# Performance work log

Hardware: AMD Instinct MI355X
Metric: run time of the kernel (lower is better)

The kernel has to match this reference:

```python
import jax, jax.numpy as jnp
import numpy as np

K = 5          # kernel_size per pseudo-dim
KK = K * K     # 25 weight slots (dim=2)
NUM_GRAPHS = 64


def spline_conv(x, src, dst, pseudo, W, root, bias):
    """SplineConv, degree-1 open B-spline, dim=2, aggr='mean', root weight + bias.
    x: [N, I], pseudo: [E, 2] in [0,1], W: [KK, I, O], root: [I, O], bias: [O].
    """
    N = x.shape[0]
    E = src.shape[0]
    O = W.shape[-1]
    # degree-1 open spline: v = u * (K-1); linear interpolation between knots
    v = pseudo * (K - 1)                      # [E, 2]
    bot = jnp.floor(v)
    frac = v - bot                            # [E, 2]
    bot = bot.astype(jnp.int32)
    # precompute per-node transform for every kernel slot: [N, KK, O] -> flat [N*KK, O]
    Xk = jnp.einsum('ni,kio->nko', x, W).reshape(N * KK, O)
    msg = jnp.zeros((E, O), x.dtype)
    for s0 in (0, 1):
        b0 = frac[:, 0] if s0 else 1.0 - frac[:, 0]
        i0 = jnp.clip(bot[:, 0] + s0, 0, K - 1)
        for s1 in (0, 1):
            b1 = frac[:, 1] if s1 else 1.0 - frac[:, 1]
            i1 = jnp.clip(bot[:, 1] + s1, 0, K - 1)
            flat = src * KK + i0 * K + i1     # [E] gather index into Xk
            msg = msg + (b0 * b1)[:, None] * Xk[flat]
    # mean aggregation over incoming edges
    agg = jax.ops.segment_sum(msg, dst, num_segments=N)
    deg = jax.ops.segment_sum(jnp.ones((E,), x.dtype), dst, num_segments=N)
    agg = agg / jnp.maximum(deg, 1.0)[:, None]
    return agg + x @ root + bias


def batch_average(x, batch, num_graphs):
    s = jax.ops.segment_sum(x, batch, num_segments=num_graphs)
    c = jax.ops.segment_sum(jnp.ones((x.shape[0],), x.dtype), batch, num_segments=num_graphs)
    return s / jnp.maximum(c, 1.0)[:, None]


def setup_inputs() -> dict:
    key = jax.random.key(0)
    ks = jax.random.split(key, 16)
    N, E = 30000, 600000
    x = jax.random.normal(ks[0], (N, 8), dtype=jnp.float32)
    edge_index = jax.random.randint(ks[1], (2, E), 0, N, dtype=jnp.int64)
    pseudo = jax.random.uniform(ks[2], (E, 2), dtype=jnp.float32)
    batch = jnp.sort(jax.random.randint(ks[3], (N,), 0, NUM_GRAPHS, dtype=jnp.int64))

    def glorot(k, shape):
        fan = shape[-2] + shape[-1]
        return jax.random.normal(k, shape, dtype=jnp.float32) * np.sqrt(2.0 / fan)

    return {
        'x': x, 'edge_index': edge_index, 'pseudo': pseudo, 'batch': batch,
        'W1': glorot(ks[4], (KK, 8, 32)),   'root1': glorot(ks[5], (8, 32)),   'b1': jnp.zeros((32,), jnp.float32),
        'W2': glorot(ks[6], (KK, 32, 64)),  'root2': glorot(ks[7], (32, 64)),  'b2': jnp.zeros((64,), jnp.float32),
        'W3': glorot(ks[8], (KK, 64, 124)), 'root3': glorot(ks[9], (64, 124)), 'b3': jnp.zeros((124,), jnp.float32),
        'fc_w': glorot(ks[10], (124, 30)),  'fc_b': jnp.zeros((30,), jnp.float32),
    }


def reference(x, edge_index, pseudo, batch,
              W1, root1, b1, W2, root2, b2, W3, root3, b3, fc_w, fc_b):
    src = edge_index[0].astype(jnp.int32)
    dst = edge_index[1].astype(jnp.int32)
    batch32 = batch.astype(jnp.int32)
    h = jax.nn.elu(spline_conv(x, src, dst, pseudo, W1, root1, b1))
    h = jax.nn.elu(spline_conv(h, src, dst, pseudo, W2, root2, b2))
    h = jax.nn.elu(spline_conv(h, src, dst, pseudo, W3, root3, b3))
    g = batch_average(h, batch32, NUM_GRAPHS)        # [G, 124]
    # dropout is identity in eval mode
    logits = g @ fc_w + fc_b                         # [G, 30]
    return jax.nn.log_softmax(logits, axis=-1)
```

## Files before the change

kernel.cpp:

```cpp
#include <hip/hip_runtime.h>
#include <cstdint>
#include <cstddef>

#define KKSLOTS 25

typedef __attribute__((ext_vector_type(8))) short short8;
typedef __attribute__((ext_vector_type(4))) float f32x4;
typedef __attribute__((ext_vector_type(4))) unsigned short us4;

__device__ __forceinline__ unsigned short f2bf(float f) {
    unsigned u = __float_as_uint(f);
    u += 0x7FFF + ((u >> 16) & 1);
    return (unsigned short)(u >> 16);
}
__device__ __forceinline__ float bf2f(unsigned short b) {
    return __uint_as_float((unsigned)b << 16);
}

__global__ void csr_count_kernel(const int* __restrict__ dst, int* __restrict__ cnt, int E) {
    int e = blockIdx.x * blockDim.x + threadIdx.x;
    if (e < E) atomicAdd(&cnt[dst[e]], 1);
}

#define SCAN_B 256
__global__ __launch_bounds__(SCAN_B) void scan1_kernel(const int* __restrict__ cnt,
                                                       int* __restrict__ off,
                                                       int* __restrict__ bsum, int N) {
    __shared__ int tmp[SCAN_B];
    int g = blockIdx.x * SCAN_B + threadIdx.x;
    int v = (g < N) ? cnt[g] : 0;
    tmp[threadIdx.x] = v;
    __syncthreads();
    for (int d = 1; d < SCAN_B; d <<= 1) {
        int t = (threadIdx.x >= d) ? tmp[threadIdx.x - d] : 0;
        __syncthreads();
        tmp[threadIdx.x] += t;
        __syncthreads();
    }
    if (g < N) off[g] = tmp[threadIdx.x] - v;
    if (threadIdx.x == SCAN_B - 1) bsum[blockIdx.x] = tmp[threadIdx.x];
}

__global__ __launch_bounds__(SCAN_B) void scan2_kernel(int* __restrict__ bsum, int nb) {
    __shared__ int tmp[SCAN_B];
    int v = (threadIdx.x < nb) ? bsum[threadIdx.x] : 0;
    tmp[threadIdx.x] = v;
    __syncthreads();
    for (int d = 1; d < SCAN_B; d <<= 1) {
        int t = (threadIdx.x >= d) ? tmp[threadIdx.x - d] : 0;
        __syncthreads();
        tmp[threadIdx.x] += t;
        __syncthreads();
    }
    if (threadIdx.x < nb) bsum[threadIdx.x] = tmp[threadIdx.x] - v;
}

__global__ void scan3_kernel(int* __restrict__ off, const int* __restrict__ bsum, int N) {
    int g = blockIdx.x * SCAN_B + threadIdx.x;
    if (g < N) off[g] += bsum[blockIdx.x];
}

__global__ void csr_fill_kernel(const int* __restrict__ src, const int* __restrict__ dst,
                                const float* __restrict__ pseudo,
                                int* __restrict__ off, int4* __restrict__ rec, int E) {
    int e = blockIdx.x * blockDim.x + threadIdx.x;
    if (e >= E) return;
    int d = dst[e];
    int p = atomicAdd(&off[d], 1);
    float v0 = pseudo[2 * e + 0] * 4.0f;
    float v1 = pseudo[2 * e + 1] * 4.0f;
    float fl0 = floorf(v0), fl1 = floorf(v1);
    float f0 = v0 - fl0, f1 = v1 - fl1;
    int b0 = (int)fl0, b1 = (int)fl1;
    int i0a = min(max(b0, 0), 4),     i1a = min(max(b1, 0), 4);
    int i0b = min(max(b0 + 1, 0), 4), i1b = min(max(b1 + 1, 0), 4);
    int s00 = i0a * 5 + i1a;
    int s01 = i0a * 5 + i1b;
    int s10 = i0b * 5 + i1a;
    int s11 = i0b * 5 + i1b;
    int packed = s00 | (s01 << 5) | (s10 << 10) | (s11 << 15);
    int4 r;
    r.x = src[e];
    r.y = packed;
    r.z = __float_as_int(f0);
    r.w = __float_as_int(f1);
    rec[p] = r;
}

__global__ void to_bf16_kernel(const float* __restrict__ in, unsigned short* __restrict__ out, int n) {
    int i = blockIdx.x * 256 + threadIdx.x;
    if (i < n) out[i] = f2bf(in[i]);
}

template<int KP, int I, int O, int OP>
__global__ void build_wt_kernel(const float* __restrict__ W, const float* __restrict__ root,
                                unsigned short* __restrict__ WT) {
    int idx = blockIdx.x * 256 + threadIdx.x;
    if (idx >= OP * KP) return;
    int o = idx / KP, k = idx - o * KP;
    float v = 0.0f;
    if (o < O) {
        if (k < KKSLOTS * I) v = W[(size_t)k * O + o];
        else if (k < (KKSLOTS + 1) * I) v = root[(size_t)(k - KKSLOTS * I) * O + o];
    }
    WT[idx] = f2bf(v);
}

template<int I>
__device__ __forceinline__ void edge_add(float* la, int lane, int4 r,
                                         const unsigned short* __restrict__ xb) {
    float f0 = __int_as_float(r.z), f1 = __int_as_float(r.w);
    float g0 = 1.0f - f0, g1 = 1.0f - f1;
    int pk = r.y;
    if constexpr (I == 64) {
        float xv = bf2f(xb[(size_t)r.x * 64 + lane]);
        la[((pk      ) & 31) * 64 + lane] += g0 * g1 * xv;
        la[((pk >> 5 ) & 31) * 64 + lane] += g0 * f1 * xv;
        la[((pk >> 10) & 31) * 64 + lane] += f0 * g1 * xv;
        la[((pk >> 15) & 31) * 64 + lane] += f0 * f1 * xv;
    } else if constexpr (I == 32) {
        int ch = lane & 31, half = lane >> 5;
        float xv = bf2f(xb[(size_t)r.x * 32 + ch]);
        float wA = half ? f0 : g0;
        int sh = half * 10;
        int sA = (pk >> sh) & 31, sB = (pk >> (sh + 5)) & 31;
        la[sA * 32 + ch] += wA * g1 * xv;
        la[sB * 32 + ch] += wA * f1 * xv;
    } else {
        int ch = lane & 7, corner = (lane >> 3) & 3;
        if (lane < 32) {
            float xv = bf2f(xb[(size_t)r.x * 8 + ch]);
            int s = (pk >> (corner * 5)) & 31;
            float w = ((corner & 2) ? f0 : g0) * ((corner & 1) ? f1 : g1);
            la[s * 8 + ch] += w * xv;
        }
    }
}

template<int I, int KP>
__global__ __launch_bounds__(256) void seg_accum_kernel(
        const unsigned short* __restrict__ xb, const int4* __restrict__ rec,
        const int* __restrict__ off, unsigned short* __restrict__ accB,
        int nlo, int nhi) {
    constexpr int SLOTS = KKSLOTS * I;
    __shared__ float la_all[4][SLOTS];
    int wline = threadIdx.x >> 6, lane = threadIdx.x & 63;
    float* la = la_all[wline];
    int wid = blockIdx.x * 4 + wline;
    int nwt = gridDim.x << 2;

    int e_lo = (nlo == 0) ? 0 : off[nlo - 1];
    int e_hi = off[nhi - 1];
    long long span = (long long)e_hi - e_lo;
    int t0 = e_lo + (int)(span * wid / nwt);
    int t1 = e_lo + (int)(span * (wid + 1) / nwt);

    int ns, ne;
    {   int lo = nlo, hi = nhi;
        while (lo < hi) { int m = (lo + hi) >> 1; if (off[m] > t0) hi = m; else lo = m + 1; }
        ns = (wid == 0) ? nlo : lo; }
    {   int lo = nlo, hi = nhi;
        while (lo < hi) { int m = (lo + hi) >> 1; if (off[m] > t1) hi = m; else lo = m + 1; }
        ne = (wid == nwt - 1) ? nhi : lo; }
    if (ns >= ne) return;

    for (int t = lane; t < SLOTS; t += 64) la[t] = 0.0f;
    int j = (ns == 0) ? 0 : off[ns - 1];
    for (int n = ns; n < ne; ++n) {
        int je = off[n];
        int jstart = j;
        while (j + 4 <= je) {
            int4 r0 = rec[j], r1 = rec[j + 1], r2 = rec[j + 2], r3 = rec[j + 3];
            edge_add<I>(la, lane, r0, xb);
            edge_add<I>(la, lane, r1, xb);
            edge_add<I>(la, lane, r2, xb);
            edge_add<I>(la, lane, r3, xb);
            j += 4;
        }
        while (j < je) { edge_add<I>(la, lane, rec[j], xb); ++j; }

        float dinv = 1.0f / fmaxf((float)(je - jstart), 1.0f);
        unsigned short* drow = accB + (size_t)(n - nlo) * KP;
        for (int t = lane; t < SLOTS; t += 64) drow[t] = f2bf(la[t] * dinv);
        for (int t = SLOTS + lane; t < KP; t += 64) {
            int ii = t - SLOTS;
            drow[t] = (ii < I) ? xb[(size_t)n * I + ii] : (unsigned short)0;
        }
        for (int t = lane; t < SLOTS; t += 64) la[t] = 0.0f;
    }
}

template<int KP, int O, int OP>
__global__ __launch_bounds__(256) void contract_mfma_kernel(
        const unsigned short* __restrict__ accB, const unsigned short* __restrict__ WT,
        const float* __restrict__ bias, unsigned short* __restrict__ hout,
        int nlo, int nhi) {
    constexpr int NF = OP / 16;
    constexpr int LDW = 40;
    __shared__ unsigned short wTl[OP][LDW];
    int tid = threadIdx.x;
    int wv = tid >> 6, lane = tid & 63;
    int quad = lane >> 4, l16 = lane & 15;
    int n0 = nlo + blockIdx.x * 64;

    int an = n0 + wv * 16 + l16;
    int arow = min(an, nhi - 1) - nlo;

    f32x4 acc[NF];
    #pragma unroll
    for (int t = 0; t < NF; ++t) acc[t] = (f32x4){0.0f, 0.0f, 0.0f, 0.0f};

    for (int k0 = 0; k0 < KP; k0 += 32) {
        for (int t = tid; t < OP * 8; t += 256) {
            int o = t >> 3;
            int kk = (t & 7) * 4;
            *(us4*)&wTl[o][kk] = *(const us4*)&WT[(size_t)o * KP + k0 + kk];
        }
        __syncthreads();
        short8 a = *(const short8*)(accB + (size_t)arow * KP + k0 + quad * 8);
        #pragma unroll
        for (int t = 0; t < NF; ++t) {
            short8 b = *(const short8*)&wTl[t * 16 + l16][quad * 8];
            acc[t] = __builtin_amdgcn_mfma_f32_16x16x32_bf16(a, b, acc[t], 0, 0, 0);
        }
        __syncthreads();
    }

    #pragma unroll
    for (int t = 0; t < NF; ++t) {
        int o = t * 16 + l16;
        if (o >= O) continue;
        float bs = bias[o];
        #pragma unroll
        for (int r = 0; r < 4; ++r) {
            int n = n0 + wv * 16 + quad * 4 + r;
            if (n >= nhi) continue;
            float v = acc[t][r] + bs;
            v = (v > 0.0f) ? v : expm1f(v);
            hout[(size_t)n * O + o] = f2bf(v);
        }
    }
}

#define GS_CH 128
__global__ __launch_bounds__(128) void graph_reduce_kernel(
        const unsigned short* __restrict__ h3, const int* __restrict__ batch,
        float* __restrict__ g, int N) {
    int o = threadIdx.x;
    if (o >= 124) return;
    int n0 = blockIdx.x * GS_CH;
    int n1 = min(n0 + GS_CH, N);
    float local = 0.0f;
    int cur_b = batch[n0];
    for (int n = n0; n < n1; ++n) {
        int b = batch[n];
        if (b != cur_b) {
            atomicAdd(&g[cur_b * 124 + o], local);
            local = 0.0f;
            cur_b = b;
        }
        local += bf2f(h3[(size_t)n * 124 + o]);
    }
    atomicAdd(&g[cur_b * 124 + o], local);
}

__global__ __launch_bounds__(256) void batch_count_kernel(
        const int* __restrict__ batch, float* __restrict__ cnt, int N) {
    __shared__ int hist[64];
    int tid = threadIdx.x;
    if (tid < 64) hist[tid] = 0;
    __syncthreads();
    int n = blockIdx.x * blockDim.x + tid;
    if (n < N) atomicAdd(&hist[batch[n]], 1);
    __syncthreads();
    if (tid < 64 && hist[tid] > 0) atomicAdd(&cnt[tid], (float)hist[tid]);
}

__global__ void head_kernel(const float* __restrict__ g, const float* __restrict__ cnt,
                            const float* __restrict__ fcw, const float* __restrict__ fcb,
                            float* __restrict__ out) {
    __shared__ float logits[32];
    __shared__ float red[2];
    int b = blockIdx.x;
    int o = threadIdx.x;
    float c = fmaxf(cnt[b], 1.0f);
    if (o < 30) {
        float a = fcb[o];
        for (int i = 0; i < 124; ++i)
            a = fmaf(g[b * 124 + i] / c, fcw[i * 30 + o], a);
        logits[o] = a;
    }
    __syncthreads();
    if (o == 0) {
        float m = -1e30f;
        for (int j = 0; j < 30; ++j) m = fmaxf(m, logits[j]);
        float s = 0.0f;
        for (int j = 0; j < 30; ++j) s += expf(logits[j] - m);
        red[0] = m;
        red[1] = logf(s);
    }
    __syncthreads();
    if (o < 30) out[b * 30 + o] = logits[o] - red[0] - red[1];
}

template<int I, int O, int OP>
static void run_layer(const unsigned short* hb, const unsigned short* WT, const float* bias,
                      unsigned short* hout, unsigned short* accB,
                      const int4* rec, const int* off,
                      int N, size_t avail, hipStream_t stream) {
    constexpr int KP = ((26 * I + 31) / 32) * 32;
    size_t perNode = (size_t)KP * 2;
    size_t maxNodesS = avail / perNode;
    int maxNodes = (maxNodesS > (size_t)N) ? N : (int)maxNodesS;
    if (maxNodes < 64) maxNodes = 64;
    for (int nlo = 0; nlo < N; nlo += maxNodes) {
        int nhi = nlo + maxNodes;
        if (nhi > N) nhi = N;
        int cn = nhi - nlo;
        seg_accum_kernel<I, KP><<<1024, 256, 0, stream>>>(hb, rec, off, accB, nlo, nhi);
        contract_mfma_kernel<KP, O, OP><<<(cn + 63) / 64, 256, 0, stream>>>(
            accB, WT, bias, hout, nlo, nhi);
    }
}

extern "C" void kernel_launch(void* const* d_in, const int* in_sizes, int n_in,
                              void* d_out, int out_size, void* d_ws, size_t ws_size,
                              hipStream_t stream) {
    const float* x      = (const float*)d_in[0];
    const int*   ei     = (const int*)  d_in[1];
    const float* pseudo = (const float*)d_in[2];
    const int*   batch  = (const int*)  d_in[3];
    const float* W1 = (const float*)d_in[4];
    const float* r1 = (const float*)d_in[5];
    const float* b1 = (const float*)d_in[6];
    const float* W2 = (const float*)d_in[7];
    const float* r2 = (const float*)d_in[8];
    const float* b2 = (const float*)d_in[9];
    const float* W3 = (const float*)d_in[10];
    const float* r3 = (const float*)d_in[11];
    const float* b3 = (const float*)d_in[12];
    const float* fcw = (const float*)d_in[13];
    const float* fcb = (const float*)d_in[14];

    int N = in_sizes[0] / 8;
    int E = in_sizes[1] / 2;
    const int* srcp = ei;
    const int* dstp = ei + E;

    constexpr int KP1 = 224, KP2 = 832, KP3 = 1664;

    char* p = (char*)d_ws;
    unsigned short* xb  = (unsigned short*)p; p += (size_t)N * 8 * 2;
    unsigned short* h1  = (unsigned short*)p; p += (size_t)N * 32 * 2;
    unsigned short* h2  = (unsigned short*)p; p += (size_t)N * 64 * 2;
    unsigned short* h3  = (unsigned short*)p; p += (size_t)N * 124 * 2;
    float* gbuf = (float*)p; p += 64 * 124 * 4;
    float* cntF = (float*)p; p += 256;
    int*   cntI = (int*)p;   p += ((size_t)N * 4 + 15) & ~15ULL;
    int*   off  = (int*)p;   p += ((size_t)N * 4 + 15) & ~15ULL;
    int*   bsum = (int*)p;   p += SCAN_B * 4;
    int4*  rec  = (int4*)p;  p += (size_t)E * 16;
    unsigned short* WT1 = (unsigned short*)p; p += (size_t)32  * KP1 * 2;
    unsigned short* WT2 = (unsigned short*)p; p += (size_t)64  * KP2 * 2;
    unsigned short* WT3 = (unsigned short*)p; p += (size_t)128 * KP3 * 2;
    unsigned short* accB = (unsigned short*)p;
    size_t used = (size_t)(p - (char*)d_ws);
    size_t avail = (ws_size > used) ? (ws_size - used) : 0;

    hipMemsetAsync(gbuf, 0, 64 * 124 * 4 + 256 + (((size_t)N * 4 + 15) & ~15ULL), stream);

    int nb_scan = (N + SCAN_B - 1) / SCAN_B;
    csr_count_kernel<<<(E + 255) / 256, 256, 0, stream>>>(dstp, cntI, E);
    scan1_kernel<<<nb_scan, SCAN_B, 0, stream>>>(cntI, off, bsum, N);
    scan2_kernel<<<1, SCAN_B, 0, stream>>>(bsum, nb_scan);
    scan3_kernel<<<nb_scan, SCAN_B, 0, stream>>>(off, bsum, N);
    csr_fill_kernel<<<(E + 255) / 256, 256, 0, stream>>>(srcp, dstp, pseudo, off, rec, E);

    to_bf16_kernel<<<(N * 8 + 255) / 256, 256, 0, stream>>>(x, xb, N * 8);
    build_wt_kernel<KP1, 8,  32,  32 ><<<(32  * KP1 + 255) / 256, 256, 0, stream>>>(W1, r1, WT1);
    build_wt_kernel<KP2, 32, 64,  64 ><<<(64  * KP2 + 255) / 256, 256, 0, stream>>>(W2, r2, WT2);
    build_wt_kernel<KP3, 64, 124, 128><<<(128 * KP3 + 255) / 256, 256, 0, stream>>>(W3, r3, WT3);

    run_layer<8,  32,  32 >(xb, WT1, b1, h1, accB, rec, off, N, avail, stream);
    run_layer<32, 64,  64 >(h1, WT2, b2, h2, accB, rec, off, N, avail, stream);
    run_layer<64, 124, 128>(h2, WT3, b3, h3, accB, rec, off, N, avail, stream);

    graph_reduce_kernel<<<(N + GS_CH - 1) / GS_CH, 128, 0, stream>>>(h3, batch, gbuf, N);
    batch_count_kernel<<<(N + 255) / 256, 256, 0, stream>>>(batch, cntF, N);
    head_kernel<<<64, 64, 0, stream>>>(gbuf, cntF, fcw, fcb, (float*)d_out);
}
```

Before: 509.7 us.

## Drop LDS weight staging in MFMA contraction and split output columns across grid

The contraction kernel no longer stages weight tiles through shared memory with two barriers per K step. Each lane now loads its B fragment straight from global memory, relying on L2/L1 caching of the small weight matrix. The output dimension is also split across a second grid dimension (SPLIT=2) to launch more blocks and cut per-block accumulator registers. The cost is that every block rereads its A rows once per split, and the direct B loads are uncoalesced and no longer shared between waves.

```diff
diff --git a/kernel.cpp b/kernel.cpp
--- a/kernel.cpp
+++ b/kernel.cpp
@@ -190,45 +190,41 @@
     }
 }
 
-template<int KP, int O, int OP>
+template<int KP, int O, int OP, int SPLIT>
 __global__ __launch_bounds__(256) void contract_mfma_kernel(
         const unsigned short* __restrict__ accB, const unsigned short* __restrict__ WT,
         const float* __restrict__ bias, unsigned short* __restrict__ hout,
         int nlo, int nhi) {
-    constexpr int NF = OP / 16;
-    constexpr int LDW = 40;
-    __shared__ unsigned short wTl[OP][LDW];
+    constexpr int OSUB = OP / SPLIT;
+    constexpr int NF = OSUB / 16;
     int tid = threadIdx.x;
     int wv = tid >> 6, lane = tid & 63;
     int quad = lane >> 4, l16 = lane & 15;
     int n0 = nlo + blockIdx.x * 64;
+    int ob = blockIdx.y * OSUB;
 
     int an = n0 + wv * 16 + l16;
     int arow = min(an, nhi - 1) - nlo;
+    const unsigned short* ap = accB + (size_t)arow * KP + quad * 8;
+    const unsigned short* bp = WT + (size_t)(ob + l16) * KP + quad * 8;
 
     f32x4 acc[NF];
     #pragma unroll
     for (int t = 0; t < NF; ++t) acc[t] = (f32x4){0.0f, 0.0f, 0.0f, 0.0f};
 
+    #pragma unroll 4
     for (int k0 = 0; k0 < KP; k0 += 32) {
-        for (int t = tid; t < OP * 8; t += 256) {
-            int o = t >> 3;
-            int kk = (t & 7) * 4;
-            *(us4*)&wTl[o][kk] = *(const us4*)&WT[(size_t)o * KP + k0 + kk];
-        }
-        __syncthreads();
-        short8 a = *(const short8*)(accB + (size_t)arow * KP + k0 + quad * 8);
+        short8 a = *(const short8*)(ap + k0);
         #pragma unroll
         for (int t = 0; t < NF; ++t) {
-            short8 b = *(const short8*)&wTl[t * 16 + l16][quad * 8];
+            short8 b = *(const short8*)(bp + (size_t)t * 16 * KP + k0);
             acc[t] = __builtin_amdgcn_mfma_f32_16x16x32_bf16(a, b, acc[t], 0, 0, 0);
         }
-        __syncthreads();
     }
 
     #pragma unroll
     for (int t = 0; t < NF; ++t) {
-        int o = t * 16 + l16;
+        int o = ob + t * 16 + l16;
         if (o >= O) continue;
         float bs = bias[o];
         #pragma unroll
@@ -303,7 +299,7 @@
     if (o < 30) out[b * 30 + o] = logits[o] - red[0] - red[1];
 }
 
-template<int I, int O, int OP>
+template<int I, int O, int OP, int SPLIT>
 static void run_layer(const unsigned short* hb, const unsigned short* WT, const float* bias,
                       unsigned short* hout, unsigned short* accB,
                       const int4* rec, const int* off,
@@ -318,7 +314,7 @@
         if (nhi > N) nhi = N;
         int cn = nhi - nlo;
         seg_accum_kernel<I, KP><<<1024, 256, 0, stream>>>(hb, rec, off, accB, nlo, nhi);
-        contract_mfma_kernel<KP, O, OP><<<(cn + 63) / 64, 256, 0, stream>>>(
+        contract_mfma_kernel<KP, O, OP, SPLIT><<<dim3((cn + 63) / 64, SPLIT), 256, 0, stream>>>(
             accB, WT, bias, hout, nlo, nhi);
     }
 }
@@ -381,9 +377,9 @@
     build_wt_kernel<KP2, 32, 64,  64 ><<<(64  * KP2 + 255) / 256, 256, 0, stream>>>(W2, r2, WT2);
     build_wt_kernel<KP3, 64, 124, 128><<<(128 * KP3 + 255) / 256, 256, 0, stream>>>(W3, r3, WT3);
 
-    run_layer<8,  32,  32 >(xb, WT1, b1, h1, accB, rec, off, N, avail, stream);
-    run_layer<32, 64,  64 >(h1, WT2, b2, h2, accB, rec, off, N, avail, stream);
-    run_layer<64, 124, 128>(h2, WT3, b3, h3, accB, rec, off, N, avail, stream);
+    run_layer<8,  32,  32,  2>(xb, WT1, b1, h1, accB, rec, off, N, avail, stream);
+    run_layer<32, 64,  64,  2>(h1, WT2, b2, h2, accB, rec, off, N, avail, stream);
+    run_layer<64, 124, 128, 2>(h2, WT3, b3, h3, accB, rec, off, N, avail, stream);
 
     graph_reduce_kernel<<<(N + GS_CH - 1) / GS_CH, 128, 0, stream>>>(h3, batch, gbuf, N);
     batch_count_kernel<<<(N + 255) / 256, 256, 0, stream>>>(batch, cntF, N);
```

Result: slower. 563.0 us (+10.5%).

## Restructure MFMA contraction with split-K waves, direct weight loads, and padded output

Applied to the files above, without the earlier changes.

Rewrites the contraction kernel so each block handles 16 nodes. The four waves split work two ways over K halves and two ways over output halves, and read weight fragments straight from global memory with register double-buffering instead of staging them through LDS with per-step barriers. Partial sums from the two K halves are combined through a shared-memory float buffer before bias, ELU and vectorized bf16 stores. The layer-3 output is padded to 128 columns and KP is rounded to a multiple of 64 so the K range divides evenly. This trades more blocks and repeated global reads of the weights (which must hit in cache) for fewer synchronizations and better latency hiding.

```diff
diff --git a/kernel.cpp b/kernel.cpp
--- a/kernel.cpp
+++ b/kernel.cpp
@@ -191,53 +191,77 @@
 }
 
 template<int KP, int O, int OP>
-__global__ __launch_bounds__(256) void contract_mfma_kernel(
+__global__ __launch_bounds__(256, 4) void contract_mfma_kernel(
         const unsigned short* __restrict__ accB, const unsigned short* __restrict__ WT,
         const float* __restrict__ bias, unsigned short* __restrict__ hout,
         int nlo, int nhi) {
-    constexpr int NF = OP / 16;
-    constexpr int LDW = 40;
-    __shared__ unsigned short wTl[OP][LDW];
+    constexpr int OSUB = OP / 2;
+    constexpr int NF = OSUB / 16;
+    constexpr int SH = (KP / 32) / 2;
+    __shared__ float pl[2][16][OP];
+
     int tid = threadIdx.x;
     int wv = tid >> 6, lane = tid & 63;
+    int kh = wv & 1, oh = wv >> 1;
     int quad = lane >> 4, l16 = lane & 15;
-    int n0 = nlo + blockIdx.x * 64;
-
-    int an = n0 + wv * 16 + l16;
+    int n0 = nlo + blockIdx.x * 16;
+
+    int an = n0 + l16;
     int arow = min(an, nhi - 1) - nlo;
+    const unsigned short* ap = accB + (size_t)arow * KP + kh * (SH * 32) + quad * 8;
+    const unsigned short* bp = WT + (size_t)(oh * OSUB + l16) * KP + kh * (SH * 32) + quad * 8;
 
     f32x4 acc[NF];
     #pragma unroll
     for (int t = 0; t < NF; ++t) acc[t] = (f32x4){0.0f, 0.0f, 0.0f, 0.0f};
 
-    for (int k0 = 0; k0 < KP; k0 += 32) {
-        for (int t = tid; t < OP * 8; t += 256) {
-            int o = t >> 3;
-            int kk = (t & 7) * 4;
-            *(us4*)&wTl[o][kk] = *(const us4*)&WT[(size_t)o * KP + k0 + kk];
-        }
-        __syncthreads();
-        short8 a = *(const short8*)(accB + (size_t)arow * KP + k0 + quad * 8);
+    short8 a_c = *(const short8*)ap;
+    short8 b_c[NF];
+    #pragma unroll
+    for (int t = 0; t < NF; ++t) b_c[t] = *(const short8*)(bp + (size_t)t * 16 * KP);
+
+    #pragma unroll 2
+    for (int s = 1; s < SH; ++s) {
+        short8 a_n = *(const short8*)(ap + s * 32);
+        short8 b_n[NF];
         #pragma unroll
-        for (int t = 0; t < NF; ++t) {
-            short8 b = *(const short8*)&wTl[t * 16 + l16][quad * 8];
-            acc[t] = __builtin_amdgcn_mfma_f32_16x16x32_bf16(a, b, acc[t], 0, 0, 0);
-        }
-        __syncthreads();
-    }
+        for (int t = 0; t < NF; ++t) b_n[t] = *(const short8*)(bp + (size_t)t * 16 * KP + s * 32);
+        #pragma unroll
+        for (int t = 0; t < NF; ++t)
+            acc[t] = __builtin_amdgcn_mfma_f32_16x16x32_bf16(a_c, b_c[t], acc[t], 0, 0, 0);
+        a_c = a_n;
+        #pragma unroll
+        for (int t = 0; t < NF; ++t) b_c[t] = b_n[t];
+    }
+    #pragma unroll
+    for (int t = 0; t < NF; ++t)
+        acc[t] = __builtin_amdgcn_mfma_f32_16x16x32_bf16(a_c, b_c[t], acc[t], 0, 0, 0);
 
     #pragma unroll
     for (int t = 0; t < NF; ++t) {
-        int o = t * 16 + l16;
-        if (o >= O) continue;
-        float bs = bias[o];
+        int o = oh * OSUB + t * 16 + l16;
         #pragma unroll
-        for (int r = 0; r < 4; ++r) {
-            int n = n0 + wv * 16 + quad * 4 + r;
-            if (n >= nhi) continue;
-            float v = acc[t][r] + bs;
-            v = (v > 0.0f) ? v : expm1f(v);
-            hout[(size_t)n * O + o] = f2bf(v);
+        for (int r = 0; r < 4; ++r)
+            pl[kh][quad * 4 + r][o] = acc[t][r];
+    }
+    __syncthreads();
+
+    constexpr int GPN = OP / 8;
+    if (tid < 16 * GPN) {
+        int node = tid / GPN;
+        int o0 = (tid - node * GPN) * 8;
+        int n = n0 + node;
+        if (n < nhi) {
+            short8 rv;
+            #pragma unroll
+            for (int j = 0; j < 8; ++j) {
+                int o = o0 + j;
+                float v = pl[0][node][o] + pl[1][node][o];
+                v += (o < O) ? bias[o] : 0.0f;
+                v = (v > 0.0f) ? v : expm1f(v);
+                rv[j] = (short)f2bf(v);
+            }
+            *(short8*)(hout + (size_t)n * OP + o0) = rv;
         }
     }
 }
@@ -259,7 +283,7 @@
             local = 0.0f;
             cur_b = b;
         }
-        local += bf2f(h3[(size_t)n * 124 + o]);
+        local += bf2f(h3[(size_t)n * 128 + o]);
     }
     atomicAdd(&g[cur_b * 124 + o], local);
 }
@@ -308,17 +332,18 @@
                       unsigned short* hout, unsigned short* accB,
                       const int4* rec, const int* off,
                       int N, size_t avail, hipStream_t stream) {
-    constexpr int KP = ((26 * I + 31) / 32) * 32;
+    constexpr int KP = ((26 * I + 63) / 64) * 64;
     size_t perNode = (size_t)KP * 2;
     size_t maxNodesS = avail / perNode;
     int maxNodes = (maxNodesS > (size_t)N) ? N : (int)maxNodesS;
-    if (maxNodes < 64) maxNodes = 64;
+    maxNodes &= ~15;
+    if (maxNodes < 16) maxNodes = 16;
     for (int nlo = 0; nlo < N; nlo += maxNodes) {
         int nhi = nlo + maxNodes;
         if (nhi > N) nhi = N;
         int cn = nhi - nlo;
         seg_accum_kernel<I, KP><<<1024, 256, 0, stream>>>(hb, rec, off, accB, nlo, nhi);
-        contract_mfma_kernel<KP, O, OP><<<(cn + 63) / 64, 256, 0, stream>>>(
+        contract_mfma_kernel<KP, O, OP><<<(cn + 15) / 16, 256, 0, stream>>>(
             accB, WT, bias, hout, nlo, nhi);
     }
 }
@@ -347,13 +372,13 @@
     const int* srcp = ei;
     const int* dstp = ei + E;
 
-    constexpr int KP1 = 224, KP2 = 832, KP3 = 1664;
+    constexpr int KP1 = 256, KP2 = 832, KP3 = 1664;
 
     char* p = (char*)d_ws;
     unsigned short* xb  = (unsigned short*)p; p += (size_t)N * 8 * 2;
     unsigned short* h1  = (unsigned short*)p; p += (size_t)N * 32 * 2;
     unsigned short* h2  = (unsigned short*)p; p += (size_t)N * 64 * 2;
-    unsigned short* h3  = (unsigned short*)p; p += (size_t)N * 124 * 2;
+    unsigned short* h3  = (unsigned short*)p; p += (size_t)N * 128 * 2;
     float* gbuf = (float*)p; p += 64 * 124 * 4;
     float* cntF = (float*)p; p += 256;
     int*   cntI = (int*)p;   p += ((size_t)N * 4 + 15) & ~15ULL;
```

After: 573.5 us. +12.5%, slower.

## Double-buffer MFMA contraction with direct global-to-LDS loads and XOR swizzle

Applied to the files above, without the earlier changes.

Rewrites the contraction kernel to stage both the A tile (aggregated features) and the B tile (weights) into LDS with global_load_lds, double-buffered so the next k-slice loads while MFMAs run on the current one. The block grows to 512 threads, with the output columns split across two wave groups, and an XOR swizzle is applied to avoid LDS bank conflicts. The h3 row stride is padded to 128, and node chunks are rounded to multiples of 64. This trades more LDS use and lower occupancy for hidden load latency and one fewer barrier per k step.

```diff
diff --git a/kernel.cpp b/kernel.cpp
--- a/kernel.cpp
+++ b/kernel.cpp
@@ -15,6 +15,12 @@
 }
 __device__ __forceinline__ float bf2f(unsigned short b) {
     return __uint_as_float((unsigned)b << 16);
+}
+
+__device__ __forceinline__ void gload16(const void* g, void* l) {
+    __builtin_amdgcn_global_load_lds(
+        (const __attribute__((address_space(1))) unsigned*)g,
+        (__attribute__((address_space(3))) unsigned*)l, 16, 0, 0);
 }
 
 __global__ void csr_count_kernel(const int* __restrict__ dst, int* __restrict__ cnt, int E) {
@@ -191,36 +197,65 @@
 }
 
 template<int KP, int O, int OP>
-__global__ __launch_bounds__(256) void contract_mfma_kernel(
+__global__ __launch_bounds__(512) void contract_mfma_kernel(
         const unsigned short* __restrict__ accB, const unsigned short* __restrict__ WT,
         const float* __restrict__ bias, unsigned short* __restrict__ hout,
         int nlo, int nhi) {
-    constexpr int NF = OP / 16;
-    constexpr int LDW = 40;
-    __shared__ unsigned short wTl[OP][LDW];
+    constexpr int OSUB = OP / 2;
+    constexpr int NF = OSUB / 16;
+    constexpr int NS = KP / 32;
+    constexpr int BT = OP * 64;
+    constexpr int AT = 64 * 64;
+    __shared__ __attribute__((aligned(16))) char Bt[2][BT];
+    __shared__ __attribute__((aligned(16))) char At[2][AT];
+
     int tid = threadIdx.x;
     int wv = tid >> 6, lane = tid & 63;
+    int ng = wv & 3, oh = wv >> 2;
     int quad = lane >> 4, l16 = lane & 15;
     int n0 = nlo + blockIdx.x * 64;
 
-    int an = n0 + wv * 16 + l16;
-    int arow = min(an, nhi - 1) - nlo;
+    const char* WTc = (const char*)WT;
+    const char* ACc = (const char*)accB;
+    int pB = tid * 16;
+    int rowB = pB >> 6;
+    int colB = (pB & 63) ^ (((rowB >> 1) & 3) << 4);
+    const char* bsrc = WTc + (size_t)rowB * (KP * 2) + colB;
+    int pA = tid * 16;
+    int rowA = pA >> 6;
+    int arowA = min(n0 + rowA, nhi - 1) - nlo;
+    int colA = (pA & 63) ^ (((rowA >> 1) & 3) << 4);
+    const char* asrc = ACc + (size_t)arowA * (KP * 2) + colA;
+
+    int rA = ng * 16 + l16;
+    int aoff = rA * 64 + ((quad ^ ((rA >> 1) & 3)) << 4);
+    int boff[NF];
+    #pragma unroll
+    for (int t = 0; t < NF; ++t) {
+        int rB = oh * OSUB + t * 16 + l16;
+        boff[t] = rB * 64 + ((quad ^ ((rB >> 1) & 3)) << 4);
+    }
 
     f32x4 acc[NF];
     #pragma unroll
     for (int t = 0; t < NF; ++t) acc[t] = (f32x4){0.0f, 0.0f, 0.0f, 0.0f};
 
-    for (int k0 = 0; k0 < KP; k0 += 32) {
-        for (int t = tid; t < OP * 8; t += 256) {
-            int o = t >> 3;
-            int kk = (t & 7) * 4;
-            *(us4*)&wTl[o][kk] = *(const us4*)&WT[(size_t)o * KP + k0 + kk];
-        }
-        __syncthreads();
-        short8 a = *(const short8*)(accB + (size_t)arow * KP + k0 + quad * 8);
+    auto STAGE = [&](int buf, int k0) {
+        int kb = k0 * 2;
+        if (pB < BT) gload16(bsrc + kb, &Bt[buf][wv << 10]);
+        if (pA < AT) gload16(asrc + kb, &At[buf][wv << 10]);
+    };
+
+    STAGE(0, 0);
+    __syncthreads();
+
+    for (int s = 0; s < NS; ++s) {
+        int cur = s & 1;
+        if (s + 1 < NS) STAGE(cur ^ 1, (s + 1) * 32);
+        short8 a = *(const short8*)(At[cur] + aoff);
         #pragma unroll
         for (int t = 0; t < NF; ++t) {
-            short8 b = *(const short8*)&wTl[t * 16 + l16][quad * 8];
+            short8 b = *(const short8*)(Bt[cur] + boff[t]);
             acc[t] = __builtin_amdgcn_mfma_f32_16x16x32_bf16(a, b, acc[t], 0, 0, 0);
         }
         __syncthreads();
@@ -228,16 +263,16 @@
 
     #pragma unroll
     for (int t = 0; t < NF; ++t) {
-        int o = t * 16 + l16;
+        int o = oh * OSUB + t * 16 + l16;
         if (o >= O) continue;
         float bs = bias[o];
         #pragma unroll
         for (int r = 0; r < 4; ++r) {
-            int n = n0 + wv * 16 + quad * 4 + r;
+            int n = n0 + ng * 16 + quad * 4 + r;
             if (n >= nhi) continue;
             float v = acc[t][r] + bs;
             v = (v > 0.0f) ? v : expm1f(v);
-            hout[(size_t)n * O + o] = f2bf(v);
+            hout[(size_t)n * OP + o] = f2bf(v);
         }
     }
 }
@@ -259,7 +294,7 @@
             local = 0.0f;
             cur_b = b;
         }
-        local += bf2f(h3[(size_t)n * 124 + o]);
+        local += bf2f(h3[(size_t)n * 128 + o]);
     }
     atomicAdd(&g[cur_b * 124 + o], local);
 }
@@ -312,13 +347,14 @@
     size_t perNode = (size_t)KP * 2;
     size_t maxNodesS = avail / perNode;
     int maxNodes = (maxNodesS > (size_t)N) ? N : (int)maxNodesS;
+    maxNodes &= ~63;
     if (maxNodes < 64) maxNodes = 64;
     for (int nlo = 0; nlo < N; nlo += maxNodes) {
         int nhi = nlo + maxNodes;
         if (nhi > N) nhi = N;
         int cn = nhi - nlo;
         seg_accum_kernel<I, KP><<<1024, 256, 0, stream>>>(hb, rec, off, accB, nlo, nhi);
-        contract_mfma_kernel<KP, O, OP><<<(cn + 63) / 64, 256, 0, stream>>>(
+        contract_mfma_kernel<KP, O, OP><<<(cn + 63) / 64, 512, 0, stream>>>(
             accB, WT, bias, hout, nlo, nhi);
     }
 }
@@ -353,7 +389,7 @@
     unsigned short* xb  = (unsigned short*)p; p += (size_t)N * 8 * 2;
     unsigned short* h1  = (unsigned short*)p; p += (size_t)N * 32 * 2;
     unsigned short* h2  = (unsigned short*)p; p += (size_t)N * 64 * 2;
-    unsigned short* h3  = (unsigned short*)p; p += (size_t)N * 124 * 2;
+    unsigned short* h3  = (unsigned short*)p; p += (size_t)N * 128 * 2;
     float* gbuf = (float*)p; p += 64 * 124 * 4;
     float* cntF = (float*)p; p += 256;
     int*   cntI = (int*)p;   p += ((size_t)N * 4 + 15) & ~15ULL;
```

Result: no change. 518.3 us (+1.7%).
